# Kernel tuning notes

Measured on AMD Instinct MI355X. Metric: run time of the kernel, lower is better.

Reference implementation:

```python
import jax, jax.numpy as jnp
import numpy as np

D_MODEL = 1024
N_HEADS = 16
DEPTH = D_MODEL // N_HEADS  # 64
GATE_DIM = 512
B, S = 2, 2048


def setup_inputs() -> dict:
    key = jax.random.key(0)
    ks = jax.random.split(key, 16)
    sd = lambda fan_in: 1.0 / np.sqrt(fan_in)
    inp = {
        "v": jax.random.normal(ks[0], (B, S, D_MODEL), jnp.float32),
        "k": jax.random.normal(ks[1], (B, S, D_MODEL), jnp.float32),
        "q": jax.random.normal(ks[2], (B, S, D_MODEL), jnp.float32),
        # padding mask: 1.0 => masked out (added as -1e9)
        "mask": (jax.random.uniform(ks[3], (B, 1, 1, S)) < 0.1).astype(jnp.float32),
        "Wq": jax.random.normal(ks[4], (D_MODEL, D_MODEL), jnp.float32) * sd(D_MODEL),
        "bq": jnp.zeros((D_MODEL,), jnp.float32),
        "Wk": jax.random.normal(ks[5], (D_MODEL, D_MODEL), jnp.float32) * sd(D_MODEL),
        "bk": jnp.zeros((D_MODEL,), jnp.float32),
        "Wv": jax.random.normal(ks[6], (D_MODEL, D_MODEL), jnp.float32) * sd(D_MODEL),
        "bv": jnp.zeros((D_MODEL,), jnp.float32),
        "Wgk": jax.random.normal(ks[7], (DEPTH, GATE_DIM), jnp.float32) * sd(DEPTH),
        "bgk": jnp.zeros((GATE_DIM,), jnp.float32),
        "Wgq": jax.random.normal(ks[8], (DEPTH, GATE_DIM), jnp.float32) * sd(DEPTH),
        "bgq": jnp.zeros((GATE_DIM,), jnp.float32),
        "Wm": jax.random.normal(ks[9], (GATE_DIM, 2), jnp.float32) * sd(GATE_DIM),
        "bm": jnp.zeros((2,), jnp.float32),
        "Wo": jax.random.normal(ks[10], (D_MODEL, D_MODEL), jnp.float32) * sd(D_MODEL),
        "bo": jnp.zeros((D_MODEL,), jnp.float32),
    }
    return inp


def _split_heads(x):
    # (B, S, d_model) -> (B, H, S, depth)
    b, s, _ = x.shape
    return x.reshape(b, s, N_HEADS, DEPTH).transpose(0, 2, 1, 3)


def reference(v, k, q, mask, Wq, bq, Wk, bk, Wv, bv,
              Wgk, bgk, Wgq, bgq, Wm, bm, Wo, bo):
    qh = _split_heads(q @ Wq + bq)  # (B,H,S,D)
    kh = _split_heads(k @ Wk + bk)
    vh = _split_heads(v @ Wv + bv)

    # gated scaled dot-product attention (is_self=True path, gate_dim=512)
    gk = kh @ Wgk + bgk                      # (B,H,S,512)
    gq = qh @ Wgq + bgq                      # (B,H,S,512)
    M = jax.nn.sigmoid((gk * gq) @ Wm + bm)  # (B,H,S,2)
    qh = qh * M[..., 0:1]
    kh = kh * M[..., 1:2]

    scale = 1.0 / jnp.sqrt(jnp.float32(DEPTH))
    logits = jnp.einsum("bhqd,bhkd->bhqk", qh, kh) * scale
    logits = logits + mask * -1e9
    attn = jax.nn.softmax(logits, axis=-1)           # (B,H,Sq,Sk)
    out = jnp.einsum("bhqk,bhkd->bhqd", attn, vh)    # (B,H,S,D)

    out = out.transpose(0, 2, 1, 3).reshape(out.shape[0], -1, D_MODEL)
    out = out @ Wo + bo
    return out, attn
```

## Files before the change

kernel.cpp:

```cpp
#include <hip/hip_runtime.h>
#include <hip/hip_bf16.h>
#include <cstdint>
#include <cstddef>

typedef __attribute__((ext_vector_type(8))) short short8;
typedef __attribute__((ext_vector_type(4))) short short4v;
typedef __attribute__((ext_vector_type(4))) float f32x4;

#define M4      4194304ull
#define OUT_ELE 4194304ull

static __device__ __forceinline__ short f2bf(float f) {
  __hip_bfloat16 h = __float2bfloat16(f);
  union { __hip_bfloat16 b; short s; } u; u.b = h; return u.s;
}
static __device__ __forceinline__ float bf2f(short s) {
  union { short s; __hip_bfloat16 b; } u; u.s = s; return __bfloat162float(u.b);
}
static __device__ __forceinline__ void split2(float v, short &hi, short &lo) {
  hi = f2bf(v);
  lo = f2bf(v - bf2f(hi));
}

typedef void __attribute__((address_space(1)))* gas1_t;
typedef void __attribute__((address_space(3)))* las3_t;
static __device__ __forceinline__ void gload16(const void* g, void* l) {
  __builtin_amdgcn_global_load_lds((gas1_t)(void*)g, (las3_t)l, 16, 0, 0);
}

__global__ void k_split_inputs(const float* __restrict__ q, const float* __restrict__ k,
                               const float* __restrict__ v,
                               short* __restrict__ xh, short* __restrict__ xl) {
  int z = blockIdx.y;
  const float* src = (z == 0) ? q : ((z == 1) ? k : v);
  size_t i = ((size_t)blockIdx.x * blockDim.x + threadIdx.x) * 4;
  float4 f = *(const float4*)(src + i);
  size_t o = (size_t)z * M4 + i;
  short h0,l0,h1,l1,h2,l2,h3,l3;
  split2(f.x,h0,l0); split2(f.y,h1,l1); split2(f.z,h2,l2); split2(f.w,h3,l3);
  short4v hv = {h0,h1,h2,h3}, lv = {l0,l1,l2,l3};
  *(short4v*)(xh + o) = hv;
  *(short4v*)(xl + o) = lv;
}

__global__ void k_prep_w(const float* __restrict__ Wq, const float* __restrict__ Wk,
                         const float* __restrict__ Wv, const float* __restrict__ Wo,
                         short* __restrict__ wth, short* __restrict__ wtl) {
  int z = blockIdx.z;
  const float* W = (z==0)?Wq:((z==1)?Wk:((z==2)?Wv:Wo));
  __shared__ float tile[32][33];
  int n0 = blockIdx.x * 32, k0 = blockIdx.y * 32;
  int tx = threadIdx.x & 31, ty = threadIdx.x >> 5;
  #pragma unroll
  for (int s = 0; s < 4; ++s)
    tile[ty + 8*s][tx] = W[(size_t)(k0 + ty + 8*s) * 1024 + n0 + tx];
  __syncthreads();
  size_t zb = (size_t)z * 1048576;
  #pragma unroll
  for (int s = 0; s < 4; ++s) {
    float vv = tile[tx][ty + 8*s];
    short hi, lo; split2(vv, hi, lo);
    size_t idx = zb + (size_t)(n0 + ty + 8*s) * 1024 + k0 + tx;
    wth[idx] = hi; wtl[idx] = lo;
  }
}

__global__ void k_gateprep(const float* __restrict__ Wgk, const float* __restrict__ Wgq,
                           const float* __restrict__ Wm,
                           const float* __restrict__ bgk, const float* __restrict__ bgq,
                           const float* __restrict__ bm,
                           float* __restrict__ A, float* __restrict__ U,
                           float* __restrict__ Wvec, float* __restrict__ Cc) {
  int t = blockIdx.x / 65;
  int d = blockIdx.x % 65;
  bool isW = (d == 64);
  __shared__ float T[128 * 65];
  __shared__ float sj[512];
  __shared__ float red[256];
  int tid = threadIdx.x;
  for (int j = tid; j < 512; j += 256)
    sj[j] = Wm[(size_t)j * 2 + t] * (isW ? bgk[j] : Wgk[(size_t)d * 512 + j]);
  __syncthreads();
  int grp = tid >> 6, e = tid & 63;
  float acc = 0.f;
  for (int c = 0; c < 4; ++c) {
    int j0 = c * 128;
    __syncthreads();
    for (int it = 0; it < 32; ++it) {
      int lin = it * 256 + tid;
      int jj = lin & 127, ee = lin >> 7;
      T[jj * 65 + ee] = Wgq[(size_t)ee * 512 + j0 + jj];
    }
    __syncthreads();
    for (int jj = grp * 32; jj < grp * 32 + 32; ++jj)
      acc = fmaf(sj[j0 + jj], T[jj * 65 + e], acc);
  }
  red[tid] = acc;
  __syncthreads();
  if (grp == 0) {
    float r = red[e] + red[64 + e] + red[128 + e] + red[192 + e];
    if (isW) Wvec[t * 64 + e] = r;
    else     A[(size_t)t * 4096 + d * 64 + e] = r;
  }
  if (tid == 0) {
    float s = 0.f;
    for (int j = 0; j < 512; ++j) s += sj[j] * bgq[j];
    if (isW) Cc[t] = s + bm[t];
    else     U[t * 64 + d] = s;
  }
}

template<int EPI>
__global__ __launch_bounds__(256) void k_gemm(
    const short* __restrict__ Ah_g, const short* __restrict__ Al_g,
    const short* __restrict__ Bh_g, const short* __restrict__ Bl_g,
    const float* __restrict__ b0, const float* __restrict__ b1, const float* __restrict__ b2,
    float* __restrict__ Cout, short* __restrict__ Oh, short* __restrict__ Ol,
    short* __restrict__ vt_h, short* __restrict__ vt_l) {
  const int K = 1024;
  int z = blockIdx.z;
  const short* Ah = Ah_g + (size_t)z * M4;
  const short* Al = Al_g + (size_t)z * M4;
  const short* Bh = Bh_g + (size_t)z * 1048576;
  const short* Bl = Bl_g + (size_t)z * 1048576;
  const float* bias = (z == 0) ? b0 : ((z == 1) ? b1 : b2);
  int lin = blockIdx.y * 8 + blockIdx.x;
  int wl = (lin & 7) * 32 + (lin >> 3);
  int m0 = (wl >> 3) * 128, n0 = (wl & 7) * 128;
  __shared__ __align__(16) short As_h[4096], As_l[4096], Bs_h[4096], Bs_l[4096];
  int tid = threadIdx.x;
  int l = tid & 63, w = tid >> 6;
  int wr = w >> 1, wc = w & 1;
  int ar = l & 15, ko = (l >> 4) * 8;
  f32x4 acc[4][4];
  #pragma unroll
  for (int m = 0; m < 4; ++m)
    #pragma unroll
    for (int n = 0; n < 4; ++n) acc[m][n] = {0.f,0.f,0.f,0.f};
  for (int kk = 0; kk < K; kk += 32) {
    __syncthreads();
    #pragma unroll
    for (int p = 0; p < 2; ++p) {
      int g = p * 256 + tid;
      int row = g >> 2, gc = (g & 3) * 8;
      size_t as = (size_t)(m0 + row) * K + kk + gc;
      size_t bs = (size_t)(n0 + row) * K + kk + gc;
      int ldb = g * 16;
      gload16(&Ah[as], (char*)As_h + ldb);
      gload16(&Al[as], (char*)As_l + ldb);
      gload16(&Bh[bs], (char*)Bs_h + ldb);
      gload16(&Bl[bs], (char*)Bs_l + ldb);
    }
    __syncthreads();
    short8 aH[4], aL[4], bH[4], bL[4];
    #pragma unroll
    for (int m = 0; m < 4; ++m) {
      int r = (wr * 64 + m * 16 + ar) * 32 + ko;
      aH[m] = *(short8*)&As_h[r];
      aL[m] = *(short8*)&As_l[r];
    }
    #pragma unroll
    for (int n = 0; n < 4; ++n) {
      int r = (wc * 64 + n * 16 + ar) * 32 + ko;
      bH[n] = *(short8*)&Bs_h[r];
      bL[n] = *(short8*)&Bs_l[r];
    }
    #pragma unroll
    for (int m = 0; m < 4; ++m)
      #pragma unroll
      for (int n = 0; n < 4; ++n) {
        acc[m][n] = __builtin_amdgcn_mfma_f32_16x16x32_bf16(aH[m], bH[n], acc[m][n], 0, 0, 0);
        acc[m][n] = __builtin_amdgcn_mfma_f32_16x16x32_bf16(aH[m], bL[n], acc[m][n], 0, 0, 0);
        acc[m][n] = __builtin_amdgcn_mfma_f32_16x16x32_bf16(aL[m], bH[n], acc[m][n], 0, 0, 0);
      }
  }
  #pragma unroll
  for (int m = 0; m < 4; ++m)
    #pragma unroll
    for (int n = 0; n < 4; ++n) {
      int row0 = m0 + wr * 64 + m * 16 + (l >> 4) * 4;
      int col  = n0 + wc * 64 + n * 16 + ar;
      if (EPI == 1) {
        #pragma unroll
        for (int i = 0; i < 4; ++i)
          Cout[(size_t)(row0 + i) * 1024 + col] = acc[m][n][i] + bias[col];
      } else if (z == 2) {
        int bq = row0 >> 11, s = row0 & 2047, hh = col >> 6, dd = col & 63;
        size_t vb = (((size_t)(bq * 16 + hh)) * 64 + dd) * 2048 + s;
        short4v hv, lv;
        #pragma unroll
        for (int i = 0; i < 4; ++i) {
          float vv = acc[m][n][i] + bias[col];
          short hi, lo; split2(vv, hi, lo);
          hv[i] = hi; lv[i] = lo;
        }
        *(short4v*)&vt_h[vb] = hv;
        *(short4v*)&vt_l[vb] = lv;
      } else {
        #pragma unroll
        for (int i = 0; i < 4; ++i) {
          int row = row0 + i;
          int bq = row >> 11, s = row & 2047, hh = col >> 6, dd = col & 63;
          size_t idx = (size_t)z * M4 + (((size_t)(bq * 16 + hh)) * 2048 + s) * 64 + dd;
          float vv = acc[m][n][i] + bias[col];
          short hi, lo; split2(vv, hi, lo);
          Oh[idx] = hi; Ol[idx] = lo;
        }
      }
    }
}

__global__ void k_gate(short* __restrict__ qh_h, short* __restrict__ qh_l,
                       short* __restrict__ kh_h, short* __restrict__ kh_l,
                       const float* __restrict__ A, const float* __restrict__ U,
                       const float* __restrict__ Wvec, const float* __restrict__ Cc) {
  __shared__ float A0s[4096], A1s[4096];
  __shared__ float rowk[4][64];
  int tid = threadIdx.x, w = tid >> 6, l = tid & 63;
  for (int i = tid; i < 4096; i += 256) { A0s[i] = A[i]; A1s[i] = A[4096 + i]; }
  __syncthreads();
  float u0 = U[l], u1 = U[64 + l];
  float w0 = Wvec[l], w1 = Wvec[64 + l];
  float c0 = Cc[0], c1 = Cc[1];
  for (int rr = 0; rr < 16; ++rr) {
    size_t row = (size_t)blockIdx.x * 64 + w * 16 + rr;
    size_t base = row * 64 + l;
    float qv = bf2f(qh_h[base]) + bf2f(qh_l[base]);
    float kv = bf2f(kh_h[base]) + bf2f(kh_l[base]);
    rowk[w][l] = kv;
    float y0 = 0.f, y1 = 0.f;
    for (int dd = 0; dd < 64; ++dd) {
      float kd = rowk[w][dd];
      y0 = fmaf(kd, A0s[dd * 64 + l], y0);
      y1 = fmaf(kd, A1s[dd * 64 + l], y1);
    }
    float p0 = y0 * qv + u0 * kv + w0 * qv;
    float p1 = y1 * qv + u1 * kv + w1 * qv;
    #pragma unroll
    for (int mm = 1; mm < 64; mm <<= 1) { p0 += __shfl_xor(p0, mm); p1 += __shfl_xor(p1, mm); }
    p0 += c0; p1 += c1;
    float M0 = 1.f / (1.f + expf(-p0));
    float M1 = 1.f / (1.f + expf(-p1));
    short hi, lo;
    split2(qv * M0, hi, lo); qh_h[base] = hi; qh_l[base] = lo;
    split2(kv * M1, hi, lo); kh_h[base] = hi; kh_l[base] = lo;
  }
}

__global__ __launch_bounds__(512, 4) void k_attn(
    const short* __restrict__ ph_h, const short* __restrict__ ph_l,
    const short* __restrict__ vt_h, const short* __restrict__ vt_l,
    const float* __restrict__ mask,
    float* __restrict__ attn, short* __restrict__ mh_h, short* __restrict__ mh_l) {
  int bid = blockIdx.x;
  int xcd = bid & 7, slot = bid >> 3;
  int bh = (xcd << 2) | (slot >> 4);
  int s0 = (slot & 15) << 7;
  int b = bh >> 4, h = bh & 15;
  int tid = threadIdx.x, w = tid >> 6, l = tid & 63;
  int ar = l & 15, hi4 = l >> 4, a7 = ar & 7;
  __shared__ __align__(16) short Ksh[2][4096];
  __shared__ __align__(16) short Ksl[2][4096];
  __shared__ __align__(16) short Vsh[2][4096];
  __shared__ __align__(16) short Vsl[2][4096];
  __shared__ __align__(16) short Pb[8][1024];

  const short* kh_h = ph_h + M4;
  const short* kh_l = ph_l + M4;
  const char* gKh = (const char*)kh_h + (size_t)bh * 2048 * 128;
  const char* gKl = (const char*)kh_l + (size_t)bh * 2048 * 128;
  const char* gVh = (const char*)vt_h + (size_t)bh * 64 * 4096;
  const char* gVl = (const char*)vt_l + (size_t)bh * 64 * 4096;
  const float* maskp = mask + (size_t)b * 2048;

  int rowbase = s0 + w * 16;
  size_t qbase = ((size_t)bh * 2048 + rowbase + ar) * 64 + (size_t)hi4 * 8;
  short8 aH0 = *(const short8*)&ph_h[qbase];
  short8 aH1 = *(const short8*)&ph_h[qbase + 32];
  short8 aL0 = *(const short8*)&ph_l[qbase];
  short8 aL1 = *(const short8*)&ph_l[qbase + 32];

  #define STAGE_K(tile, buf) {                                          \
    const char* th_ = gKh + (size_t)(tile) * 8192;                      \
    const char* tl_ = gKl + (size_t)(tile) * 8192;                      \
    int col_ = tid >> 3, j_ = tid & 7;                                  \
    int gs_ = col_ * 128 + ((j_ ^ (col_ & 7)) << 4);                    \
    gload16(th_ + gs_, (char*)&Ksh[buf][0] + tid * 16);                 \
    gload16(tl_ + gs_, (char*)&Ksl[buf][0] + tid * 16);                 \
  }

  #define STAGE_V(tile, buf) {                                          \
    int row_ = tid >> 3, j_ = tid & 7;                                  \
    int gs_ = row_ * 4096 + (tile) * 128 + ((j_ ^ (row_ & 7)) << 4);    \
    gload16(gVh + gs_, (char*)&Vsh[buf][0] + tid * 16);                 \
    gload16(gVl + gs_, (char*)&Vsl[buf][0] + tid * 16);                 \
  }

  #define QKT(buf, tile) {                                              \
    const char* kbh_ = (const char*)&Ksh[buf][0];                       \
    const char* kbl_ = (const char*)&Ksl[buf][0];                       \
    _Pragma("unroll")                                                   \
    for (int n = 0; n < 4; ++n) {                                       \
      int colloc = n * 16 + ar;                                         \
      int cb = colloc * 128;                                            \
      short8 bH0 = *(const short8*)(kbh_ + cb + ((hi4 ^ a7) << 4));     \
      short8 bH1 = *(const short8*)(kbh_ + cb + (((hi4 + 4) ^ a7) << 4));\
      short8 bL0 = *(const short8*)(kbl_ + cb + ((hi4 ^ a7) << 4));     \
      short8 bL1 = *(const short8*)(kbl_ + cb + (((hi4 + 4) ^ a7) << 4));\
      f32x4 c = {0.f,0.f,0.f,0.f};                                      \
      c = __builtin_amdgcn_mfma_f32_16x16x32_bf16(aH0, bH0, c, 0,0,0);  \
      c = __builtin_amdgcn_mfma_f32_16x16x32_bf16(aH1, bH1, c, 0,0,0);  \
      c = __builtin_amdgcn_mfma_f32_16x16x32_bf16(aH0, bL0, c, 0,0,0);  \
      c = __builtin_amdgcn_mfma_f32_16x16x32_bf16(aH1, bL1, c, 0,0,0);  \
      c = __builtin_amdgcn_mfma_f32_16x16x32_bf16(aL0, bH0, c, 0,0,0);  \
      c = __builtin_amdgcn_mfma_f32_16x16x32_bf16(aL1, bH1, c, 0,0,0);  \
      float mv = maskp[(tile) * 64 + colloc] * -1e9f;                   \
      _Pragma("unroll")                                                 \
      for (int i = 0; i < 4; ++i) lg[n][i] = c[i] * 0.125f + mv;        \
    } }

  float ls[4] = {0.f, 0.f, 0.f, 0.f};

  STAGE_K(0, 0);
  #pragma unroll 1
  for (int t = 0; t < 32; ++t) {
    __syncthreads();
    STAGE_K((t + 1) & 31, (t + 1) & 1);
    f32x4 lg[4];
    QKT(t & 1, t);
    #pragma unroll
    for (int n = 0; n < 4; ++n)
      #pragma unroll
      for (int i = 0; i < 4; ++i) ls[i] += __expf(lg[n][i]);
  }
  #pragma unroll
  for (int mk = 1; mk < 16; mk <<= 1)
    #pragma unroll
    for (int i = 0; i < 4; ++i) ls[i] += __shfl_xor(ls[i], mk);
  float invl[4];
  #pragma unroll
  for (int i = 0; i < 4; ++i) invl[i] = 1.f / ls[i];

  f32x4 acc[4];
  #pragma unroll
  for (int dn = 0; dn < 4; ++dn) acc[dn] = {0.f,0.f,0.f,0.f};
  size_t arow = (size_t)bh * 2048 + rowbase;

  STAGE_V(0, 0);
  #pragma unroll 1
  for (int t = 0; t < 32; ++t) {
    __syncthreads();
    if (t < 31) { STAGE_K(t + 1, (t + 1) & 1); STAGE_V(t + 1, (t + 1) & 1); }
    f32x4 lg[4];
    QKT(t & 1, t);
    char* pbw = (char*)&Pb[w][0];
    #pragma unroll
    for (int n = 0; n < 4; ++n) {
      #pragma unroll
      for (int i = 0; i < 4; ++i) {
        float p = __expf(lg[n][i]) * invl[i];
        lg[n][i] = p;
        int r = hi4 * 4 + i;
        int off = (r * 128 + (n * 16 + ar) * 2) ^ ((r & 7) << 4);
        *(short*)(pbw + off) = f2bf(p);
      }
    }
    #pragma unroll
    for (int ks = 0; ks < 2; ++ks) {
      int roff = (ar * 128 + ks * 64 + hi4 * 16) ^ (a7 << 4);
      short8 pah = *(const short8*)(pbw + roff);
      #pragma unroll
      for (int dn = 0; dn < 4; ++dn) {
        int voff = (dn * 16 + ar) * 128 + ((ks * 64 + hi4 * 16) ^ (a7 << 4));
        short8 vH = *(const short8*)((const char*)&Vsh[t & 1][0] + voff);
        short8 vL = *(const short8*)((const char*)&Vsl[t & 1][0] + voff);
        acc[dn] = __builtin_amdgcn_mfma_f32_16x16x32_bf16(pah, vH, acc[dn], 0,0,0);
        acc[dn] = __builtin_amdgcn_mfma_f32_16x16x32_bf16(pah, vL, acc[dn], 0,0,0);
      }
    }
    #pragma unroll
    for (int n = 0; n < 4; ++n)
      #pragma unroll
      for (int i = 0; i < 4; ++i)
        __builtin_nontemporal_store(lg[n][i],
            &attn[(arow + hi4 * 4 + i) * 2048 + t * 64 + n * 16 + ar]);
  }
  #pragma unroll
  for (int dn = 0; dn < 4; ++dn)
    #pragma unroll
    for (int i = 0; i < 4; ++i) {
      short hh, ll; split2(acc[dn][i], hh, ll);
      size_t idx = ((size_t)b * 2048 + rowbase + hi4 * 4 + i) * 1024
                 + h * 64 + dn * 16 + ar;
      mh_h[idx] = hh; mh_l[idx] = ll;
    }
  #undef STAGE_K
  #undef STAGE_V
  #undef QKT
}

extern "C" void kernel_launch(void* const* d_in, const int* in_sizes, int n_in,
                              void* d_out, int out_size, void* d_ws, size_t ws_size,
                              hipStream_t stream) {
  const float* v    = (const float*)d_in[0];
  const float* k    = (const float*)d_in[1];
  const float* q    = (const float*)d_in[2];
  const float* mask = (const float*)d_in[3];
  const float* Wq   = (const float*)d_in[4];
  const float* bq   = (const float*)d_in[5];
  const float* Wk   = (const float*)d_in[6];
  const float* bk   = (const float*)d_in[7];
  const float* Wv   = (const float*)d_in[8];
  const float* bv   = (const float*)d_in[9];
  const float* Wgk  = (const float*)d_in[10];
  const float* bgk  = (const float*)d_in[11];
  const float* Wgq  = (const float*)d_in[12];
  const float* bgq  = (const float*)d_in[13];
  const float* Wm   = (const float*)d_in[14];
  const float* bm   = (const float*)d_in[15];
  const float* Wo   = (const float*)d_in[16];
  const float* bo   = (const float*)d_in[17];
  float* out  = (float*)d_out;
  float* attn = out + OUT_ELE;

  short* xh = (short*)attn;
  short* xl = xh + 3 * M4;

  short* wth  = (short*)d_ws;
  short* wtl  = wth + 4 * 1048576ull;
  short* ph_h = wtl + 4 * 1048576ull;
  short* ph_l = ph_h + 3 * M4;
  short* vt_h = ph_l + 3 * M4;
  short* vt_l = vt_h + M4;
  short* mh_h = vt_l + M4;
  short* mh_l = mh_h + M4;
  float* Ag   = (float*)(mh_l + M4);
  float* Ug   = Ag + 8192;
  float* Wvec = Ug + 128;
  float* Cg   = Wvec + 128;

  k_split_inputs<<<dim3(4096, 3), 256, 0, stream>>>(q, k, v, xh, xl);
  k_prep_w<<<dim3(32, 32, 4), 256, 0, stream>>>(Wq, Wk, Wv, Wo, wth, wtl);
  k_gateprep<<<130, 256, 0, stream>>>(Wgk, Wgq, Wm, bgk, bgq, bm, Ag, Ug, Wvec, Cg);
  k_gemm<0><<<dim3(8, 32, 3), 256, 0, stream>>>(xh, xl, wth, wtl, bq, bk, bv,
                                                nullptr, ph_h, ph_l, vt_h, vt_l);
  k_gate<<<1024, 256, 0, stream>>>(ph_h, ph_l, ph_h + M4, ph_l + M4, Ag, Ug, Wvec, Cg);
  k_attn<<<dim3(512), 512, 0, stream>>>(ph_h, ph_l, vt_h, vt_l, mask,
                                        attn, mh_h, mh_l);
  k_gemm<1><<<dim3(8, 32, 1), 256, 0, stream>>>(mh_h, mh_l,
                                                wth + 3 * 1048576ull, wtl + 3 * 1048576ull,
                                                bo, bo, bo, out, nullptr, nullptr,
                                                nullptr, nullptr);
}
```

Before: 551.8 us.

## Split attention row-sum pass into separate lightweight kernel

Moves the first pass of the two-pass softmax (QK^T plus exp-sum over all key tiles) into its own kernel, k_sums. That kernel uses only the K shared buffers and declares a higher occupancy bound, and it writes the inverse row sums to workspace. The main attention kernel then reads these sums and runs only the normalized P·V pass, which removes the pass-1 register and LDS pressure from it. The cost is an extra kernel launch and a small global round-trip for the sums, and QK^T is still computed twice overall.

Result: slower. 580.3 us (+5.2%).

```diff
diff --git a/kernel.cpp b/kernel.cpp
--- a/kernel.cpp
+++ b/kernel.cpp
@@ -247,10 +247,86 @@
   }
 }
 
-__global__ __launch_bounds__(512, 4) void k_attn(
+__global__ __launch_bounds__(512, 8) void k_sums(
+    const short* __restrict__ ph_h, const short* __restrict__ ph_l,
+    const float* __restrict__ mask, float* __restrict__ invl_g) {
+  int bid = blockIdx.x;
+  int xcd = bid & 7, slot = bid >> 3;
+  int bh = (xcd << 2) | (slot >> 4);
+  int s0 = (slot & 15) << 7;
+  int b = bh >> 4;
+  int tid = threadIdx.x, w = tid >> 6, l = tid & 63;
+  int ar = l & 15, hi4 = l >> 4, a7 = ar & 7;
+  __shared__ __align__(16) short Ksh[2][4096];
+  __shared__ __align__(16) short Ksl[2][4096];
+
+  const short* kh_h = ph_h + M4;
+  const short* kh_l = ph_l + M4;
+  const char* gKh = (const char*)kh_h + (size_t)bh * 2048 * 128;
+  const char* gKl = (const char*)kh_l + (size_t)bh * 2048 * 128;
+  const float* maskp = mask + (size_t)b * 2048;
+
+  int rowbase = s0 + w * 16;
+  size_t qbase = ((size_t)bh * 2048 + rowbase + ar) * 64 + (size_t)hi4 * 8;
+  short8 aH0 = *(const short8*)&ph_h[qbase];
+  short8 aH1 = *(const short8*)&ph_h[qbase + 32];
+  short8 aL0 = *(const short8*)&ph_l[qbase];
+  short8 aL1 = *(const short8*)&ph_l[qbase + 32];
+
+  #define STAGE_K(tile, buf) {                                          \
+    const char* th_ = gKh + (size_t)(tile) * 8192;                      \
+    const char* tl_ = gKl + (size_t)(tile) * 8192;                      \
+    int col_ = tid >> 3, j_ = tid & 7;                                  \
+    int gs_ = col_ * 128 + ((j_ ^ (col_ & 7)) << 4);                    \
+    gload16(th_ + gs_, (char*)&Ksh[buf][0] + tid * 16);                 \
+    gload16(tl_ + gs_, (char*)&Ksl[buf][0] + tid * 16);                 \
+  }
+
+  float ls[4] = {0.f, 0.f, 0.f, 0.f};
+
+  STAGE_K(0, 0);
+  #pragma unroll 1
+  for (int t = 0; t < 32; ++t) {
+    __syncthreads();
+    if (t < 31) STAGE_K(t + 1, (t + 1) & 1);
+    const char* kbh_ = (const char*)&Ksh[t & 1][0];
+    const char* kbl_ = (const char*)&Ksl[t & 1][0];
+    #pragma unroll
+    for (int n = 0; n < 4; ++n) {
+      int colloc = n * 16 + ar;
+      int cb = colloc * 128;
+      short8 bH0 = *(const short8*)(kbh_ + cb + ((hi4 ^ a7) << 4));
+      short8 bH1 = *(const short8*)(kbh_ + cb + (((hi4 + 4) ^ a7) << 4));
+      short8 bL0 = *(const short8*)(kbl_ + cb + ((hi4 ^ a7) << 4));
+      short8 bL1 = *(const short8*)(kbl_ + cb + (((hi4 + 4) ^ a7) << 4));
+      f32x4 c = {0.f,0.f,0.f,0.f};
+      c = __builtin_amdgcn_mfma_f32_16x16x32_bf16(aH0, bH0, c, 0,0,0);
+      c = __builtin_amdgcn_mfma_f32_16x16x32_bf16(aH1, bH1, c, 0,0,0);
+      c = __builtin_amdgcn_mfma_f32_16x16x32_bf16(aH0, bL0, c, 0,0,0);
+      c = __builtin_amdgcn_mfma_f32_16x16x32_bf16(aH1, bL1, c, 0,0,0);
+      c = __builtin_amdgcn_mfma_f32_16x16x32_bf16(aL0, bH0, c, 0,0,0);
+      c = __builtin_amdgcn_mfma_f32_16x16x32_bf16(aL1, bH1, c, 0,0,0);
+      float mv = maskp[t * 64 + colloc] * -1e9f;
+      #pragma unroll
+      for (int i = 0; i < 4; ++i) ls[i] += __expf(c[i] * 0.125f + mv);
+    }
+  }
+  #pragma unroll
+  for (int mk = 1; mk < 16; mk <<= 1)
+    #pragma unroll
+    for (int i = 0; i < 4; ++i) ls[i] += __shfl_xor(ls[i], mk);
+  if (ar == 0) {
+    #pragma unroll
+    for (int i = 0; i < 4; ++i)
+      invl_g[(size_t)bh * 2048 + rowbase + hi4 * 4 + i] = 1.f / ls[i];
+  }
+  #undef STAGE_K
+}
+
+__global__ __launch_bounds__(512, 4) void k_attn2(
     const short* __restrict__ ph_h, const short* __restrict__ ph_l,
     const short* __restrict__ vt_h, const short* __restrict__ vt_l,
-    const float* __restrict__ mask,
+    const float* __restrict__ mask, const float* __restrict__ invl_g,
     float* __restrict__ attn, short* __restrict__ mh_h, short* __restrict__ mh_l) {
   int bid = blockIdx.x;
   int xcd = bid & 7, slot = bid >> 3;
@@ -280,6 +356,11 @@
   short8 aL0 = *(const short8*)&ph_l[qbase];
   short8 aL1 = *(const short8*)&ph_l[qbase + 32];
 
+  float invl[4];
+  #pragma unroll
+  for (int i = 0; i < 4; ++i)
+    invl[i] = invl_g[(size_t)bh * 2048 + rowbase + hi4 * 4 + i];
+
   #define STAGE_K(tile, buf) {                                          \
     const char* th_ = gKh + (size_t)(tile) * 8192;                      \
     const char* tl_ = gKl + (size_t)(tile) * 8192;                      \
@@ -296,63 +377,41 @@
     gload16(gVl + gs_, (char*)&Vsl[buf][0] + tid * 16);                 \
   }
 
-  #define QKT(buf, tile) {                                              \
-    const char* kbh_ = (const char*)&Ksh[buf][0];                       \
-    const char* kbl_ = (const char*)&Ksl[buf][0];                       \
-    _Pragma("unroll")                                                   \
-    for (int n = 0; n < 4; ++n) {                                       \
-      int colloc = n * 16 + ar;                                         \
-      int cb = colloc * 128;                                            \
-      short8 bH0 = *(const short8*)(kbh_ + cb + ((hi4 ^ a7) << 4));     \
-      short8 bH1 = *(const short8*)(kbh_ + cb + (((hi4 + 4) ^ a7) << 4));\
-      short8 bL0 = *(const short8*)(kbl_ + cb + ((hi4 ^ a7) << 4));     \
-      short8 bL1 = *(const short8*)(kbl_ + cb + (((hi4 + 4) ^ a7) << 4));\
-      f32x4 c = {0.f,0.f,0.f,0.f};                                      \
-      c = __builtin_amdgcn_mfma_f32_16x16x32_bf16(aH0, bH0, c, 0,0,0);  \
-      c = __builtin_amdgcn_mfma_f32_16x16x32_bf16(aH1, bH1, c, 0,0,0);  \
-      c = __builtin_amdgcn_mfma_f32_16x16x32_bf16(aH0, bL0, c, 0,0,0);  \
-      c = __builtin_amdgcn_mfma_f32_16x16x32_bf16(aH1, bL1, c, 0,0,0);  \
-      c = __builtin_amdgcn_mfma_f32_16x16x32_bf16(aL0, bH0, c, 0,0,0);  \
-      c = __builtin_amdgcn_mfma_f32_16x16x32_bf16(aL1, bH1, c, 0,0,0);  \
-      float mv = maskp[(tile) * 64 + colloc] * -1e9f;                   \
-      _Pragma("unroll")                                                 \
-      for (int i = 0; i < 4; ++i) lg[n][i] = c[i] * 0.125f + mv;        \
-    } }
-
-  float ls[4] = {0.f, 0.f, 0.f, 0.f};
-
-  STAGE_K(0, 0);
-  #pragma unroll 1
-  for (int t = 0; t < 32; ++t) {
-    __syncthreads();
-    STAGE_K((t + 1) & 31, (t + 1) & 1);
-    f32x4 lg[4];
-    QKT(t & 1, t);
-    #pragma unroll
-    for (int n = 0; n < 4; ++n)
-      #pragma unroll
-      for (int i = 0; i < 4; ++i) ls[i] += __expf(lg[n][i]);
-  }
-  #pragma unroll
-  for (int mk = 1; mk < 16; mk <<= 1)
-    #pragma unroll
-    for (int i = 0; i < 4; ++i) ls[i] += __shfl_xor(ls[i], mk);
-  float invl[4];
-  #pragma unroll
-  for (int i = 0; i < 4; ++i) invl[i] = 1.f / ls[i];
-
   f32x4 acc[4];
   #pragma unroll
   for (int dn = 0; dn < 4; ++dn) acc[dn] = {0.f,0.f,0.f,0.f};
   size_t arow = (size_t)bh * 2048 + rowbase;
 
+  STAGE_K(0, 0);
   STAGE_V(0, 0);
   #pragma unroll 1
   for (int t = 0; t < 32; ++t) {
     __syncthreads();
     if (t < 31) { STAGE_K(t + 1, (t + 1) & 1); STAGE_V(t + 1, (t + 1) & 1); }
     f32x4 lg[4];
-    QKT(t & 1, t);
+    {
+      const char* kbh_ = (const char*)&Ksh[t & 1][0];
+      const char* kbl_ = (const char*)&Ksl[t & 1][0];
+      #pragma unroll
+      for (int n = 0; n < 4; ++n) {
+        int colloc = n * 16 + ar;
+        int cb = colloc * 128;
+        short8 bH0 = *(const short8*)(kbh_ + cb + ((hi4 ^ a7) << 4));
+        short8 bH1 = *(const short8*)(kbh_ + cb + (((hi4 + 4) ^ a7) << 4));
+        short8 bL0 = *(const short8*)(kbl_ + cb + ((hi4 ^ a7) << 4));
+        short8 bL1 = *(const short8*)(kbl_ + cb + (((hi4 + 4) ^ a7) << 4));
+        f32x4 c = {0.f,0.f,0.f,0.f};
+        c = __builtin_amdgcn_mfma_f32_16x16x32_bf16(aH0, bH0, c, 0,0,0);
+        c = __builtin_amdgcn_mfma_f32_16x16x32_bf16(aH1, bH1, c, 0,0,0);
+        c = __builtin_amdgcn_mfma_f32_16x16x32_bf16(aH0, bL0, c, 0,0,0);
+        c = __builtin_amdgcn_mfma_f32_16x16x32_bf16(aH1, bL1, c, 0,0,0);
+        c = __builtin_amdgcn_mfma_f32_16x16x32_bf16(aL0, bH0, c, 0,0,0);
+        c = __builtin_amdgcn_mfma_f32_16x16x32_bf16(aL1, bH1, c, 0,0,0);
+        float mv = maskp[t * 64 + colloc] * -1e9f;
+        #pragma unroll
+        for (int i = 0; i < 4; ++i) lg[n][i] = c[i] * 0.125f + mv;
+      }
+    }
     char* pbw = (char*)&Pb[w][0];
     #pragma unroll
     for (int n = 0; n < 4; ++n) {
@@ -396,7 +455,6 @@
     }
   #undef STAGE_K
   #undef STAGE_V
-  #undef QKT
 }
 
 extern "C" void kernel_launch(void* const* d_in, const int* in_sizes, int n_in,
@@ -438,6 +496,7 @@
   float* Ug   = Ag + 8192;
   float* Wvec = Ug + 128;
   float* Cg   = Wvec + 128;
+  float* invl_g = Cg + 64;
 
   k_split_inputs<<<dim3(4096, 3), 256, 0, stream>>>(q, k, v, xh, xl);
   k_prep_w<<<dim3(32, 32, 4), 256, 0, stream>>>(Wq, Wk, Wv, Wo, wth, wtl);
@@ -445,8 +504,9 @@
   k_gemm<0><<<dim3(8, 32, 3), 256, 0, stream>>>(xh, xl, wth, wtl, bq, bk, bv,
                                                 nullptr, ph_h, ph_l, vt_h, vt_l);
   k_gate<<<1024, 256, 0, stream>>>(ph_h, ph_l, ph_h + M4, ph_l + M4, Ag, Ug, Wvec, Cg);
-  k_attn<<<dim3(512), 512, 0, stream>>>(ph_h, ph_l, vt_h, vt_l, mask,
-                                        attn, mh_h, mh_l);
+  k_sums<<<dim3(512), 512, 0, stream>>>(ph_h, ph_l, mask, invl_g);
+  k_attn2<<<dim3(512), 512, 0, stream>>>(ph_h, ph_l, vt_h, vt_l, mask, invl_g,
+                                         attn, mh_h, mh_l);
   k_gemm<1><<<dim3(8, 32, 1), 256, 0, stream>>>(mh_h, mh_l,
                                                 wth + 3 * 1048576ull, wtl + 3 * 1048576ull,
                                                 bo, bo, bo, out, nullptr, nullptr,
```
